# Kernel tuning notes

Measured on AMD Instinct MI355X. Metric: run time of the kernel, lower is better.

## Reference

```python
import jax, jax.numpy as jnp
import numpy as np

EPS = 1e-5

def _ln(z, g, b):
    # LayerNorm over last axis (per the gammas/betas of shape (2, 3H))
    mu = jnp.mean(z, axis=-1, keepdims=True)
    var = jnp.var(z, axis=-1, keepdims=True)
    return g * (z - mu) * jax.lax.rsqrt(var + EPS) + b

def setup_inputs() -> dict:
    key = jax.random.key(0)
    ks = jax.random.split(key, 12)
    B, L, D_IN, H, A, DEPTH = 64, 512, 256, 256, 128, 4
    glorot = lambda k, sh: jax.random.normal(k, sh, jnp.float32) * np.sqrt(2.0 / (sh[0] + sh[1])).astype(np.float32)
    # variable-length prefix masks (bucketing/masking semantics of the layer)
    lengths = jax.random.randint(ks[0], (B, 1), L // 2, L + 1)
    mask = jnp.arange(L)[None, :] < lengths
    return {
        'x': jax.random.normal(ks[1], (B, L, D_IN), jnp.float32),
        'mask': mask,
        'W_emb': glorot(ks[2], (D_IN, H)),
        'b_emb': jnp.zeros((H,), jnp.float32),
        'W': glorot(ks[3], (H, 3 * H)),
        'U': glorot(ks[4], (H, 3 * H)),
        'b': jnp.zeros((3 * H,), jnp.float32),
        'W_action_1': glorot(ks[5], (H, A)),
        'U_action_1': glorot(ks[6], (H, A)),
        'b_action_1': jnp.zeros((A,), jnp.float32),
        'W_action_2': glorot(ks[7], (A, 2)),
        'b_action_2': jnp.zeros((2,), jnp.float32),
        'gammas': jnp.ones((2, 3 * H), jnp.float32),
        'betas': jnp.zeros((2, 3 * H), jnp.float32),
        'depth': DEPTH,
    }

def _run_depth(x_seq, m_seq, W, U, b, Wa1, Ua1, ba1, Wa2, ba2, gammas, betas):
    # x_seq: (L,B,H), m_seq: (L,B) bool
    H = W.shape[0]
    B = x_seq.shape[1]
    # precompute + layernorm the input projection for all steps (fusable)
    xp_all = _ln(jnp.einsum('lbh,hk->lbk', x_seq, W), gammas[0], betas[0])  # (L,B,3H)

    def step(h, inputs):
        xp, xt, mt = inputs  # (B,3H), (B,H), (B,)
        hp = _ln(h @ U, gammas[1], betas[1])
        r = jax.nn.sigmoid(xp[:, :H] + hp[:, :H] + b[:H])
        z = jax.nn.sigmoid(xp[:, H:2 * H] + hp[:, H:2 * H] + b[H:2 * H])
        hh = jnp.tanh(xp[:, 2 * H:] + r * hp[:, 2 * H:] + b[2 * H:])
        h_new = z * h + (1.0 - z) * hh
        # action-policy subnetwork (binary merge/propagate decision)
        logits = jnp.tanh(xt @ Wa1 + h @ Ua1 + ba1) @ Wa2 + ba2  # (B,2)
        pol = jax.nn.softmax(logits, axis=-1)
        act = (pol[:, 1] > pol[:, 0]) & mt
        h_out = jnp.where(mt[:, None], h_new, h)  # masked steps carry state
        return h_out, (h_out, act, pol)

    h0 = jnp.zeros((B, H), x_seq.dtype)
    _, (h_seq, act_seq, pol_seq) = jax.lax.scan(step, h0, (xp_all, x_seq, m_seq))
    return h_seq, act_seq, pol_seq

def reference(x, mask, W_emb, b_emb, W, U, b, W_action_1, U_action_1, b_action_1,
              W_action_2, b_action_2, gammas, betas, depth):
    # embedding projection, then time-major like the Theano scans
    h_seq = jnp.swapaxes(x @ W_emb + b_emb, 0, 1)  # (L,B,H)
    m_seq = jnp.swapaxes(mask, 0, 1)               # (L,B)
    actions, policies = [], []
    for _ in range(depth):  # vertical (tree-depth) scan: small fixed count
        h_new, act, pol = _run_depth(h_seq, m_seq, W, U, b,
                                     W_action_1, U_action_1, b_action_1,
                                     W_action_2, b_action_2, gammas, betas)
        actions.append(act)
        policies.append(pol)
        h_seq = h_new
        m_seq = m_seq & act  # tree collapse: only selected nodes survive upward
    output = h_seq[-1]  # (B,H) final hidden state of top layer
    action = jnp.stack(actions, 0).transpose(2, 0, 1)      # (B,depth,L)
    policy = jnp.stack(policies, 0).transpose(2, 0, 1, 3)  # (B,depth,L,2)
    return output, action, policy
```

## Files before the change

### kernel.cpp

```cpp
#include <hip/hip_runtime.h>
#include <hip/hip_bf16.h>
#include <math.h>

#define BB 64
#define LL 512
#define HH 256
#define H3 768
#define AA 128
#define NDEPTH 4
#define NROWS (LL*BB)

#define EXCH_U64_PER_CHAIN (2 * 3 * 256)

typedef float vf32x32 __attribute__((ext_vector_type(32)));

__global__ void maskcvt_kernel(const unsigned char* __restrict__ raw,
                               int* __restrict__ m)
{
    int i = blockIdx.x * blockDim.x + threadIdx.x;
    bool bytemode = (raw[1] == 1);
    int v;
    if (bytemode) v = raw[i] ? 1 : 0;
    else          v = (((const int*)raw)[i] != 0) ? 1 : 0;
    m[i] = v;
}

__global__ __launch_bounds__(512) void mkidx_kernel(
    const int* __restrict__ m,
    int* __restrict__ rowidx,
    int* __restrict__ nact)
{
    const int b    = blockIdx.x;
    const int tid  = threadIdx.x;
    const int lane = tid & 63;
    const int w    = tid >> 6;
    __shared__ int wcnt[8];
    int pred = m[b * LL + tid];
    unsigned long long bal = __ballot(pred != 0);
    int below = __popcll(bal & ((1ull << lane) - 1ull));
    if (lane == 63) wcnt[w] = __popcll(bal);
    __syncthreads();
    int woff = 0;
#pragma unroll
    for (int i = 0; i < 8; ++i) woff += (i < w) ? wcnt[i] : 0;
    if (pred) rowidx[b * LL + woff + below] = tid;
    if (tid == 511) nact[b] = woff + wcnt[7];
}

template<int MODE, int EPI>
__global__ __launch_bounds__(256) void gemm_kernel(
    const float* __restrict__ A, const float* __restrict__ Bm,
    const float* __restrict__ bias, const float* __restrict__ aux,
    float* __restrict__ C, int M, int N,
    const int* __restrict__ ridx, const int* __restrict__ nact)
{
    __shared__ float As[16][136];
    __shared__ float Bs[16][136];
    const int tid = threadIdx.x;
    const int tx = tid & 15, ty = tid >> 4;
    const int row0 = blockIdx.y * 128, col0 = blockIdx.x * 128;

    int arow0 = 0, arow1 = 0;
    if (MODE == 3) {
        const int bb = row0 >> 9;
        const int na = nact[bb];
        if ((row0 & 511) >= na) return;
        const int r0 = row0 + (tid >> 2);
        const int r1 = r0 + 64;
        const int l0 = ((r0 & 511) < na) ? ridx[r0] : 0;
        const int l1 = ((r1 & 511) < na) ? ridx[r1] : 0;
        arow0 = l0 * 64 + bb;
        arow1 = l1 * 64 + bb;
    }

    float acc[8][8];
#pragma unroll
    for (int i = 0; i < 8; ++i)
#pragma unroll
        for (int j = 0; j < 8; ++j) acc[i][j] = 0.f;

    for (int kk = 0; kk < 256; kk += 16) {
#pragma unroll
        for (int i = 0; i < 2; ++i) {
            int aid = i * 256 + tid;
            int r   = aid >> 2;
            int k4  = (aid & 3) << 2;
            int rr  = row0 + r;
            float4 v;
            if (MODE == 0) {
                v = *(const float4*)(A + rr * 256 + kk + k4);
            } else if (MODE == 1) {
                v = *(const float4*)(A + (rr & 63) * 131072 + (rr >> 6) * 256 + kk + k4);
            } else if (MODE == 2) {
                if (rr < 64) v = make_float4(0.f, 0.f, 0.f, 0.f);
                else         v = *(const float4*)(A + (rr - 64) * 256 + kk + k4);
            } else {
                int ar = i ? arow1 : arow0;
                v = *(const float4*)(A + ar * 256 + kk + k4);
            }
            As[k4 + 0][r] = v.x; As[k4 + 1][r] = v.y;
            As[k4 + 2][r] = v.z; As[k4 + 3][r] = v.w;

            int bid = i * 256 + tid;
            int bk  = bid >> 5;
            int c4  = (bid & 31) << 2;
            float4 w = *(const float4*)(Bm + (kk + bk) * N + col0 + c4);
            *(float4*)&Bs[bk][c4] = w;
        }
        __syncthreads();
#pragma unroll
        for (int k = 0; k < 16; ++k) {
            float a[8], bb2[8];
            *(float4*)&a[0]   = *(const float4*)&As[k][ty * 8];
            *(float4*)&a[4]   = *(const float4*)&As[k][ty * 8 + 4];
            *(float4*)&bb2[0] = *(const float4*)&Bs[k][tx * 8];
            *(float4*)&bb2[4] = *(const float4*)&Bs[k][tx * 8 + 4];
#pragma unroll
            for (int i = 0; i < 8; ++i)
#pragma unroll
                for (int j = 0; j < 8; ++j)
                    acc[i][j] += a[i] * bb2[j];
        }
        __syncthreads();
    }

#pragma unroll
    for (int i = 0; i < 8; ++i) {
        int row  = row0 + ty * 8 + i;
        int colb = col0 + tx * 8;
        float vout[8];
#pragma unroll
        for (int j = 0; j < 8; ++j) {
            float v = acc[i][j];
            if (EPI == 1) v += bias[colb + j];
            if (EPI == 2) v = tanhf(v + aux[row * N + colb + j]);
            vout[j] = v;
        }
        *(float4*)&C[row * N + colb]     = *(float4*)&vout[0];
        *(float4*)&C[row * N + colb + 4] = *(float4*)&vout[4];
    }
}

__global__ __launch_bounds__(256) void lnrows_kernel(
    float* __restrict__ XP, const float* __restrict__ g0,
    const float* __restrict__ b0, const float* __restrict__ gb,
    const int* __restrict__ nact)
{
    const int row = blockIdx.x;
    if ((row & 511) >= nact[row >> 9]) return;
    const int tid = threadIdx.x;
    float* p = XP + (long)row * H3;
    float v0 = p[tid], v1 = p[tid + 256], v2 = p[tid + 512];
    float s = v0 + v1 + v2;
    float q = v0 * v0 + v1 * v1 + v2 * v2;
#pragma unroll
    for (int off = 32; off >= 1; off >>= 1) {
        s += __shfl_xor(s, off);
        q += __shfl_xor(q, off);
    }
    __shared__ float rs4[4], rq4[4];
    if ((tid & 63) == 0) { rs4[tid >> 6] = s; rq4[tid >> 6] = q; }
    __syncthreads();
    float S = rs4[0] + rs4[1] + rs4[2] + rs4[3];
    float Q = rq4[0] + rq4[1] + rq4[2] + rq4[3];
    float mu  = S * (1.f / 768.f);
    float var = Q * (1.f / 768.f) - mu * mu;
    float r   = rsqrtf(var + 1e-5f);
    p[tid]       = g0[tid]       * (v0 - mu) * r + b0[tid]       + gb[tid];
    p[tid + 256] = g0[tid + 256] * (v1 - mu) * r + b0[tid + 256] + gb[tid + 256];
    p[tid + 512] = g0[tid + 512] * (v2 - mu) * r + b0[tid + 512] + gb[tid + 512];
}

__global__ __launch_bounds__(512, 2) void scan3_kernel(
    const float* __restrict__ XP,
    const float* __restrict__ U,
    const float* __restrict__ g1, const float* __restrict__ b1,
    const int* __restrict__ mask,
    float* __restrict__ Y,
    unsigned long long* __restrict__ exch,
    int seq0)
{
    const int i0   = blockIdx.x;
    const int xcd  = i0 & 7;
    const int slot = i0 >> 3;
    const int b    = xcd + 8 * (slot / 3);
    const int s    = slot % 3;
    const int tid  = threadIdx.x;
    const int kg   = tid >> 5;
    const int cg   = tid & 31;
    const int q1   = (s + 1 >= 3) ? s - 2 : s + 1;
    const int q2   = (s + 2 >= 3) ? s - 1 : s + 2;

    __shared__ float h_cur[256];
    __shared__ float part[16][256];
    __shared__ float xp_lds[768];
    __shared__ float g1s[768], b1s[768];
    __shared__ int   mk[512];
    __shared__ float reds[4], redq[4];

    vf32x32 u0v, u1v, u2v, u3v;
    {
        const volatile float* Uv = U;
        const int colbase = s * 256 + cg;
#pragma unroll
        for (int i = 0; i < 16; ++i) {
#pragma unroll
            for (int j = 0; j < 8; ++j) {
                const int f = i * 8 + j;
                float val = Uv[(kg * 16 + i) * H3 + colbase + 32 * j];
                if      (f < 32) u0v[f]      = val;
                else if (f < 64) u1v[f - 32] = val;
                else if (f < 96) u2v[f - 64] = val;
                else             u3v[f - 96] = val;
            }
        }
    }
    if (tid < 256) h_cur[tid] = 0.f;
    for (int i = tid; i < 768; i += 512) { g1s[i] = g1[i]; b1s[i] = b1[i]; }
    mk[tid] = mask[b * LL + tid];
    __syncthreads();

    unsigned long long* exb = exch + b * EXCH_U64_PER_CHAIN;
    int seq = seq0;

    for (int l = 0; l < LL; ++l) {
        if (!mk[l]) {
            if (s == 0 && tid < 64) {
                float4 hv = *(const float4*)&h_cur[tid * 4];
                *(float4*)&Y[((long)l * BB + b) * HH + tid * 4] = hv;
            }
            continue;
        }
        seq++;
        const int par = seq & 1;
        const int cs  = seq - seq0 - 1;

        float4 xr4;
        if (tid < 192) xr4 = *(const float4*)(XP + ((long)(b * LL + cs)) * H3 + tid * 4);

        float acc[8] = {0.f, 0.f, 0.f, 0.f, 0.f, 0.f, 0.f, 0.f};
#pragma unroll
        for (int i = 0; i < 4; ++i) {
            float4 hv = *(const float4*)&h_cur[kg * 16 + i * 4];
#pragma unroll
            for (int e = 0; e < 4; ++e) {
                const float hh = (e == 0) ? hv.x : (e == 1) ? hv.y
                               : (e == 2) ? hv.z : hv.w;
                const int ik = i * 4 + e;
#pragma unroll
                for (int j = 0; j < 8; ++j) {
                    const int f = ik * 8 + j;
                    const float uu = (f < 32) ? u0v[f]
                                   : (f < 64) ? u1v[f - 32]
                                   : (f < 96) ? u2v[f - 64]
                                   :            u3v[f - 96];
                    acc[j] += uu * hh;
                }
            }
        }
#pragma unroll
        for (int j = 0; j < 8; ++j)
            part[kg][cg + 32 * j] = acc[j];
        __syncthreads();

        if (tid < 192) *(float4*)&xp_lds[tid * 4] = xr4;

        float pre = 0.f, v0 = 0.f, v1 = 0.f, v2 = 0.f;
        if (tid < 256) {
            pre = part[0][tid];
#pragma unroll
            for (int gg = 1; gg < 16; ++gg) pre += part[gg][tid];

            unsigned long long pk =
                ((unsigned long long)(unsigned)seq << 32) |
                (unsigned long long)__float_as_uint(pre);
            __hip_atomic_store(&exb[(par * 3 + s) * 256 + tid], pk,
                               __ATOMIC_RELAXED, __HIP_MEMORY_SCOPE_AGENT);

            unsigned long long x1 = 0, x2 = 0;
            bool d1 = false, d2 = false;
            do {
                unsigned long long t1 =
                    __hip_atomic_load(&exb[(par * 3 + q1) * 256 + tid],
                                      __ATOMIC_RELAXED, __HIP_MEMORY_SCOPE_AGENT);
                unsigned long long t2 =
                    __hip_atomic_load(&exb[(par * 3 + q2) * 256 + tid],
                                      __ATOMIC_RELAXED, __HIP_MEMORY_SCOPE_AGENT);
                if (!d1 && (int)(t1 >> 32) == seq) { x1 = t1; d1 = true; }
                if (!d2 && (int)(t2 >> 32) == seq) { x2 = t2; d2 = true; }
            } while (!(d1 && d2));
            float w1 = __uint_as_float((unsigned)x1);
            float w2 = __uint_as_float((unsigned)x2);
            v0 = (s == 0) ? pre : ((q1 == 0) ? w1 : w2);
            v1 = (s == 1) ? pre : ((q1 == 1) ? w1 : w2);
            v2 = (s == 2) ? pre : ((q1 == 2) ? w1 : w2);

            float st = v0 + v1 + v2;
            float qt = v0 * v0 + v1 * v1 + v2 * v2;
#pragma unroll
            for (int off = 32; off >= 1; off >>= 1) {
                st += __shfl_xor(st, off);
                qt += __shfl_xor(qt, off);
            }
            if ((tid & 63) == 0) { reds[tid >> 6] = st; redq[tid >> 6] = qt; }
        }
        __syncthreads();

        if (tid < 256) {
            float S = reds[0] + reds[1] + reds[2] + reds[3];
            float Q = redq[0] + redq[1] + redq[2] + redq[3];
            float mu = S * (1.f / 768.f);
            float rs = rsqrtf(Q * (1.f / 768.f) - mu * mu + 1e-5f);
            float hp_r = g1s[tid]       * (v0 - mu) * rs + b1s[tid];
            float hp_z = g1s[256 + tid] * (v1 - mu) * rs + b1s[256 + tid];
            float hp_h = g1s[512 + tid] * (v2 - mu) * rs + b1s[512 + tid];
            float xr = xp_lds[tid], xz = xp_lds[256 + tid], xh = xp_lds[512 + tid];
            float r  = 1.f / (1.f + expf(-(xr + hp_r)));
            float z  = 1.f / (1.f + expf(-(xz + hp_z)));
            float hh = tanhf(xh + r * hp_h);
            float o  = z * h_cur[tid] + (1.f - z) * hh;
            h_cur[tid] = o;
            if (s == 0) Y[((long)l * BB + b) * HH + tid] = o;
        }
        __syncthreads();
    }
}

__global__ __launch_bounds__(256) void act_kernel(
    const float* __restrict__ T, const float* __restrict__ Wa2,
    const float* __restrict__ ba2, const int* __restrict__ mask_in,
    int* __restrict__ mask_out, float* __restrict__ act_out,
    float* __restrict__ pol_out, int d)
{
    int row  = blockIdx.x * 4 + (threadIdx.x >> 6);
    int lane = threadIdx.x & 63;
    const float* Tr = T + (long)row * AA;
    float t0 = Tr[lane], t1 = Tr[lane + 64];
    float l0 = t0 * Wa2[lane * 2]       + t1 * Wa2[(lane + 64) * 2];
    float l1 = t0 * Wa2[lane * 2 + 1]   + t1 * Wa2[(lane + 64) * 2 + 1];
#pragma unroll
    for (int off = 32; off >= 1; off >>= 1) {
        l0 += __shfl_xor(l0, off);
        l1 += __shfl_xor(l1, off);
    }
    if (lane == 0) {
        int l = row >> 6, bb = row & 63;
        l0 += ba2[0]; l1 += ba2[1];
        float m  = fmaxf(l0, l1);
        float e0 = expf(l0 - m), e1 = expf(l1 - m);
        float inv = 1.f / (e0 + e1);
        float p0 = e0 * inv, p1 = e1 * inv;
        int mt = mask_in[bb * LL + l];
        int a  = (p1 > p0) && mt;
        act_out[bb * (NDEPTH * LL) + d * LL + l] = a ? 1.f : 0.f;
        pol_out[bb * (NDEPTH * LL * 2) + d * (LL * 2) + l * 2 + 0] = p0;
        pol_out[bb * (NDEPTH * LL * 2) + d * (LL * 2) + l * 2 + 1] = p1;
        mask_out[bb * LL + l] = a;
    }
}

__global__ void final_copy_kernel(const float* __restrict__ X, float* __restrict__ out)
{
    int i = blockIdx.x * blockDim.x + threadIdx.x;
    int bb = i >> 8, j = i & 255;
    out[i] = X[((long)(LL - 1) * BB + bb) * HH + j];
}

extern "C" void kernel_launch(void* const* d_in, const int* in_sizes, int n_in,
                              void* d_out, int out_size, void* d_ws, size_t ws_size,
                              hipStream_t stream)
{
    const float* x      = (const float*)d_in[0];
    const void*  mraw   = d_in[1];
    const float* W_emb  = (const float*)d_in[2];
    const float* b_emb  = (const float*)d_in[3];
    const float* W      = (const float*)d_in[4];
    const float* U      = (const float*)d_in[5];
    const float* bias3  = (const float*)d_in[6];
    const float* Wa1    = (const float*)d_in[7];
    const float* Ua1    = (const float*)d_in[8];
    const float* ba1    = (const float*)d_in[9];
    const float* Wa2    = (const float*)d_in[10];
    const float* ba2    = (const float*)d_in[11];
    const float* gammas = (const float*)d_in[12];
    const float* betas  = (const float*)d_in[13];

    float* out = (float*)d_out;
    char*  ws  = (char*)d_ws;

    float* XP = (float*)(ws);
    float* X  = (float*)(ws + 100663296UL);
    float* Y  = (float*)(ws + 134217728UL);
    float* XA = (float*)(ws + 167772160UL);
    float* T  = XP;
    int*   m0 = (int*)(ws + 184549376UL);
    int*   m1 = (int*)(ws + 184680448UL);

    float* act_out = out + BB * HH;
    float* pol_out = act_out + BB * NDEPTH * LL;

    maskcvt_kernel<<<dim3(NROWS / 256), dim3(256), 0, stream>>>(
        (const unsigned char*)mraw, m0);

    gemm_kernel<1, 1><<<dim3(2, 256), dim3(256), 0, stream>>>(
        x, W_emb, b_emb, nullptr, X, NROWS, HH, nullptr, nullptr);

    float* Xc = X; float* Yc = Y;
    int* mc = m0; int* mn = m1;

    for (int d = 0; d < NDEPTH; ++d) {
        int* rowidx = (int*)Yc;
        int* nactp  = ((int*)Yc) + NROWS;

        mkidx_kernel<<<dim3(BB), dim3(512), 0, stream>>>(mc, rowidx, nactp);

        gemm_kernel<3, 0><<<dim3(6, 256), dim3(256), 0, stream>>>(
            Xc, W, nullptr, nullptr, XP, NROWS, H3, rowidx, nactp);
        lnrows_kernel<<<dim3(NROWS), dim3(256), 0, stream>>>(
            XP, gammas, betas, bias3, nactp);

        gemm_kernel<0, 1><<<dim3(1, 256), dim3(256), 0, stream>>>(
            Xc, Wa1, ba1, nullptr, XA, NROWS, AA, nullptr, nullptr);

        unsigned long long* exch_d = (unsigned long long*)Xc;

        scan3_kernel<<<dim3(192), dim3(512), 0, stream>>>(
            XP, U, gammas + H3, betas + H3, mc, Yc, exch_d, d << 10);

        gemm_kernel<2, 2><<<dim3(1, 256), dim3(256), 0, stream>>>(
            Yc, Ua1, nullptr, XA, T, NROWS, AA, nullptr, nullptr);
        act_kernel<<<dim3(NROWS / 4), dim3(256), 0, stream>>>(
            T, Wa2, ba2, mc, mn, act_out, pol_out, d);
        { float* tmp = Xc; Xc = Yc; Yc = tmp; }
        { int* tmp = mc; mc = mn; mn = tmp; }
    }

    final_copy_kernel<<<dim3(BB), dim3(256), 0, stream>>>(Xc, out);
}
```

Before: 3.398 ms.

## Overlap Wa1 projection with scan blocks; fuse Ua1 GEMM with action softmax

The Wa1 input projection moves into extra blocks of the scan kernel, so it runs on compute units left idle by the 192 recurrent blocks. The Ua1 GEMM is fused with the tanh/Wa2/softmax action epilogue, which removes the intermediate T buffer and a separate kernel launch. The exchange buffer gets its own workspace region because Xc is now read by the side GEMM blocks, and the spin-wait adds s_sleep backoff. Risks: the extra blocks could compete with the persistent scan blocks for residency or memory bandwidth, and the backoff could add latency to each step's exchange.

```diff
diff --git a/kernel.cpp b/kernel.cpp
--- a/kernel.cpp
+++ b/kernel.cpp
@@ -50,7 +50,7 @@
 template<int MODE, int EPI>
 __global__ __launch_bounds__(256) void gemm_kernel(
     const float* __restrict__ A, const float* __restrict__ Bm,
-    const float* __restrict__ bias, const float* __restrict__ aux,
+    const float* __restrict__ bias,
     float* __restrict__ C, int M, int N,
     const int* __restrict__ ridx, const int* __restrict__ nact)
 {
@@ -87,13 +87,8 @@
             int k4  = (aid & 3) << 2;
             int rr  = row0 + r;
             float4 v;
-            if (MODE == 0) {
-                v = *(const float4*)(A + rr * 256 + kk + k4);
-            } else if (MODE == 1) {
+            if (MODE == 1) {
                 v = *(const float4*)(A + (rr & 63) * 131072 + (rr >> 6) * 256 + kk + k4);
-            } else if (MODE == 2) {
-                if (rr < 64) v = make_float4(0.f, 0.f, 0.f, 0.f);
-                else         v = *(const float4*)(A + (rr - 64) * 256 + kk + k4);
             } else {
                 int ar = i ? arow1 : arow0;
                 v = *(const float4*)(A + ar * 256 + kk + k4);
@@ -133,7 +128,6 @@
         for (int j = 0; j < 8; ++j) {
             float v = acc[i][j];
             if (EPI == 1) v += bias[colb + j];
-            if (EPI == 2) v = tanhf(v + aux[row * N + colb + j]);
             vout[j] = v;
         }
         *(float4*)&C[row * N + colb]     = *(float4*)&vout[0];
@@ -178,25 +172,85 @@
     const int* __restrict__ mask,
     float* __restrict__ Y,
     unsigned long long* __restrict__ exch,
-    int seq0)
-{
-    const int i0   = blockIdx.x;
-    const int xcd  = i0 & 7;
-    const int slot = i0 >> 3;
-    const int b    = xcd + 8 * (slot / 3);
-    const int s    = slot % 3;
-    const int tid  = threadIdx.x;
-    const int kg   = tid >> 5;
-    const int cg   = tid & 31;
-    const int q1   = (s + 1 >= 3) ? s - 2 : s + 1;
-    const int q2   = (s + 2 >= 3) ? s - 1 : s + 2;
-
+    int seq0,
+    const float* __restrict__ Xc,
+    const float* __restrict__ Wa1,
+    const float* __restrict__ ba1,
+    float* __restrict__ XA)
+{
     __shared__ float h_cur[256];
     __shared__ float part[16][256];
     __shared__ float xp_lds[768];
     __shared__ float g1s[768], b1s[768];
     __shared__ int   mk[512];
     __shared__ float reds[4], redq[4];
+    __shared__ float As[16][136];
+    __shared__ float Bs[16][136];
+
+    const int tid = threadIdx.x;
+
+    if (blockIdx.x >= 192) {
+        const int t    = blockIdx.x - 192;
+        const int row0 = t * 128;
+        const int tx   = tid & 15;
+        const int ty4  = tid >> 4;
+        float xacc[4][8];
+#pragma unroll
+        for (int i = 0; i < 4; ++i)
+#pragma unroll
+            for (int j = 0; j < 8; ++j) xacc[i][j] = 0.f;
+
+        for (int kk = 0; kk < 256; kk += 16) {
+            {
+                int r  = tid >> 2;
+                int k4 = (tid & 3) << 2;
+                float4 v = *(const float4*)(Xc + (row0 + r) * 256 + kk + k4);
+                As[k4 + 0][r] = v.x; As[k4 + 1][r] = v.y;
+                As[k4 + 2][r] = v.z; As[k4 + 3][r] = v.w;
+            }
+            {
+                int bk = tid >> 5;
+                int c4 = (tid & 31) << 2;
+                float4 w = *(const float4*)(Wa1 + (kk + bk) * AA + c4);
+                *(float4*)&Bs[bk][c4] = w;
+            }
+            __syncthreads();
+#pragma unroll
+            for (int k = 0; k < 16; ++k) {
+                float a[4], bb2[8];
+                *(float4*)&a[0]   = *(const float4*)&As[k][ty4 * 4];
+                *(float4*)&bb2[0] = *(const float4*)&Bs[k][tx * 8];
+                *(float4*)&bb2[4] = *(const float4*)&Bs[k][tx * 8 + 4];
+#pragma unroll
+                for (int i = 0; i < 4; ++i)
+#pragma unroll
+                    for (int j = 0; j < 8; ++j)
+                        xacc[i][j] += a[i] * bb2[j];
+            }
+            __syncthreads();
+        }
+#pragma unroll
+        for (int i = 0; i < 4; ++i) {
+            int row  = row0 + ty4 * 4 + i;
+            int colb = tx * 8;
+            float vout[8];
+#pragma unroll
+            for (int j = 0; j < 8; ++j) vout[j] = xacc[i][j] + ba1[colb + j];
+            *(float4*)&XA[row * AA + colb]     = *(float4*)&vout[0];
+            *(float4*)&XA[row * AA + colb + 4] = *(float4*)&vout[4];
+        }
+        return;
+    }
+
+    const int i0   = blockIdx.x;
+    const int xcd  = i0 & 7;
+    const int slot = i0 >> 3;
+    const int b    = xcd + 8 * (slot / 3);
+    const int s    = slot % 3;
+    const int kg   = tid >> 5;
+    const int cg   = tid & 31;
+    const int q1   = (s + 1 >= 3) ? s - 2 : s + 1;
+    const int q2   = (s + 2 >= 3) ? s - 1 : s + 2;
 
     vf32x32 u0v, u1v, u2v, u3v;
     {
@@ -279,6 +333,7 @@
 
             unsigned long long x1 = 0, x2 = 0;
             bool d1 = false, d2 = false;
+            int spins = 0;
             do {
                 unsigned long long t1 =
                     __hip_atomic_load(&exb[(par * 3 + q1) * 256 + tid],
@@ -288,6 +343,7 @@
                                       __ATOMIC_RELAXED, __HIP_MEMORY_SCOPE_AGENT);
                 if (!d1 && (int)(t1 >> 32) == seq) { x1 = t1; d1 = true; }
                 if (!d2 && (int)(t2 >> 32) == seq) { x2 = t2; d2 = true; }
+                if (++spins > 8) __builtin_amdgcn_s_sleep(1);
             } while (!(d1 && d2));
             float w1 = __uint_as_float((unsigned)x1);
             float w2 = __uint_as_float((unsigned)x2);
@@ -326,36 +382,103 @@
     }
 }
 
-__global__ __launch_bounds__(256) void act_kernel(
-    const float* __restrict__ T, const float* __restrict__ Wa2,
-    const float* __restrict__ ba2, const int* __restrict__ mask_in,
-    int* __restrict__ mask_out, float* __restrict__ act_out,
-    float* __restrict__ pol_out, int d)
-{
-    int row  = blockIdx.x * 4 + (threadIdx.x >> 6);
-    int lane = threadIdx.x & 63;
-    const float* Tr = T + (long)row * AA;
-    float t0 = Tr[lane], t1 = Tr[lane + 64];
-    float l0 = t0 * Wa2[lane * 2]       + t1 * Wa2[(lane + 64) * 2];
-    float l1 = t0 * Wa2[lane * 2 + 1]   + t1 * Wa2[(lane + 64) * 2 + 1];
-#pragma unroll
-    for (int off = 32; off >= 1; off >>= 1) {
-        l0 += __shfl_xor(l0, off);
-        l1 += __shfl_xor(l1, off);
-    }
-    if (lane == 0) {
-        int l = row >> 6, bb = row & 63;
-        l0 += ba2[0]; l1 += ba2[1];
-        float m  = fmaxf(l0, l1);
-        float e0 = expf(l0 - m), e1 = expf(l1 - m);
-        float inv = 1.f / (e0 + e1);
-        float p0 = e0 * inv, p1 = e1 * inv;
-        int mt = mask_in[bb * LL + l];
-        int a  = (p1 > p0) && mt;
-        act_out[bb * (NDEPTH * LL) + d * LL + l] = a ? 1.f : 0.f;
-        pol_out[bb * (NDEPTH * LL * 2) + d * (LL * 2) + l * 2 + 0] = p0;
-        pol_out[bb * (NDEPTH * LL * 2) + d * (LL * 2) + l * 2 + 1] = p1;
-        mask_out[bb * LL + l] = a;
+__global__ __launch_bounds__(256) void gemmact_kernel(
+    const float* __restrict__ Yprev,
+    const float* __restrict__ Ua1,
+    const float* __restrict__ XA,
+    const float* __restrict__ Wa2,
+    const float* __restrict__ ba2,
+    const int* __restrict__ mask_in, int* __restrict__ mask_out,
+    float* __restrict__ act_out, float* __restrict__ pol_out, int d)
+{
+    __shared__ float As[16][136];
+    __shared__ float Bs[16][136];
+    const int tid = threadIdx.x;
+    const int tx = tid & 15, ty = tid >> 4;
+    const int row0 = blockIdx.y * 128;
+
+    float acc[8][8];
+#pragma unroll
+    for (int i = 0; i < 8; ++i)
+#pragma unroll
+        for (int j = 0; j < 8; ++j) acc[i][j] = 0.f;
+
+    for (int kk = 0; kk < 256; kk += 16) {
+#pragma unroll
+        for (int i = 0; i < 2; ++i) {
+            int aid = i * 256 + tid;
+            int r   = aid >> 2;
+            int k4  = (aid & 3) << 2;
+            int rr  = row0 + r;
+            float4 v;
+            if (rr < 64) v = make_float4(0.f, 0.f, 0.f, 0.f);
+            else         v = *(const float4*)(Yprev + (rr - 64) * 256 + kk + k4);
+            As[k4 + 0][r] = v.x; As[k4 + 1][r] = v.y;
+            As[k4 + 2][r] = v.z; As[k4 + 3][r] = v.w;
+
+            int bid = i * 256 + tid;
+            int bk  = bid >> 5;
+            int c4  = (bid & 31) << 2;
+            float4 w = *(const float4*)(Ua1 + (kk + bk) * AA + c4);
+            *(float4*)&Bs[bk][c4] = w;
+        }
+        __syncthreads();
+#pragma unroll
+        for (int k = 0; k < 16; ++k) {
+            float a[8], bb2[8];
+            *(float4*)&a[0]   = *(const float4*)&As[k][ty * 8];
+            *(float4*)&a[4]   = *(const float4*)&As[k][ty * 8 + 4];
+            *(float4*)&bb2[0] = *(const float4*)&Bs[k][tx * 8];
+            *(float4*)&bb2[4] = *(const float4*)&Bs[k][tx * 8 + 4];
+#pragma unroll
+            for (int i = 0; i < 8; ++i)
+#pragma unroll
+                for (int j = 0; j < 8; ++j)
+                    acc[i][j] += a[i] * bb2[j];
+        }
+        __syncthreads();
+    }
+
+    float p0[8], p1[8];
+#pragma unroll
+    for (int i = 0; i < 8; ++i) { p0[i] = 0.f; p1[i] = 0.f; }
+#pragma unroll
+    for (int i = 0; i < 8; ++i) {
+        int row  = row0 + ty * 8 + i;
+#pragma unroll
+        for (int j = 0; j < 8; ++j) {
+            int c   = tx * 8 + j;
+            float v = tanhf(acc[i][j] + XA[row * AA + c]);
+            p0[i] += v * Wa2[c * 2];
+            p1[i] += v * Wa2[c * 2 + 1];
+        }
+    }
+#pragma unroll
+    for (int off = 1; off < 16; off <<= 1) {
+#pragma unroll
+        for (int i = 0; i < 8; ++i) {
+            p0[i] += __shfl_xor(p0[i], off);
+            p1[i] += __shfl_xor(p1[i], off);
+        }
+    }
+    if (tx == 0) {
+#pragma unroll
+        for (int i = 0; i < 8; ++i) {
+            int row = row0 + ty * 8 + i;
+            int l   = row >> 6, bb = row & 63;
+            float l0 = p0[i] + ba2[0];
+            float l1 = p1[i] + ba2[1];
+            float m  = fmaxf(l0, l1);
+            float e0 = expf(l0 - m), e1 = expf(l1 - m);
+            float inv = 1.f / (e0 + e1);
+            float q0 = e0 * inv, q1v = e1 * inv;
+            int mt = mask_in[bb * LL + l];
+            int a  = (q1v > q0) && mt;
+            act_out[bb * (NDEPTH * LL) + d * LL + l] = a ? 1.f : 0.f;
+            pol_out[bb * (NDEPTH * LL * 2) + d * (LL * 2) + l * 2 + 0] = q0;
+            pol_out[bb * (NDEPTH * LL * 2) + d * (LL * 2) + l * 2 + 1] = q1v;
+            mask_out[bb * LL + l] = a;
+        }
     }
 }
 
@@ -392,9 +515,9 @@
     float* X  = (float*)(ws + 100663296UL);
     float* Y  = (float*)(ws + 134217728UL);
     float* XA = (float*)(ws + 167772160UL);
-    float* T  = XP;
     int*   m0 = (int*)(ws + 184549376UL);
     int*   m1 = (int*)(ws + 184680448UL);
+    unsigned long long* exch_d = (unsigned long long*)(ws + 184811520UL);
 
     float* act_out = out + BB * HH;
     float* pol_out = act_out + BB * NDEPTH * LL;
@@ -403,7 +526,7 @@
         (const unsigned char*)mraw, m0);
 
     gemm_kernel<1, 1><<<dim3(2, 256), dim3(256), 0, stream>>>(
-        x, W_emb, b_emb, nullptr, X, NROWS, HH, nullptr, nullptr);
+        x, W_emb, b_emb, X, NROWS, HH, nullptr, nullptr);
 
     float* Xc = X; float* Yc = Y;
     int* mc = m0; int* mn = m1;
@@ -415,22 +538,17 @@
         mkidx_kernel<<<dim3(BB), dim3(512), 0, stream>>>(mc, rowidx, nactp);
 
         gemm_kernel<3, 0><<<dim3(6, 256), dim3(256), 0, stream>>>(
-            Xc, W, nullptr, nullptr, XP, NROWS, H3, rowidx, nactp);
+            Xc, W, nullptr, XP, NROWS, H3, rowidx, nactp);
         lnrows_kernel<<<dim3(NROWS), dim3(256), 0, stream>>>(
             XP, gammas, betas, bias3, nactp);
 
-        gemm_kernel<0, 1><<<dim3(1, 256), dim3(256), 0, stream>>>(
-            Xc, Wa1, ba1, nullptr, XA, NROWS, AA, nullptr, nullptr);
-
-        unsigned long long* exch_d = (unsigned long long*)Xc;
-
-        scan3_kernel<<<dim3(192), dim3(512), 0, stream>>>(
-            XP, U, gammas + H3, betas + H3, mc, Yc, exch_d, d << 10);
-
-        gemm_kernel<2, 2><<<dim3(1, 256), dim3(256), 0, stream>>>(
-            Yc, Ua1, nullptr, XA, T, NROWS, AA, nullptr, nullptr);
-        act_kernel<<<dim3(NROWS / 4), dim3(256), 0, stream>>>(
-            T, Wa2, ba2, mc, mn, act_out, pol_out, d);
+        scan3_kernel<<<dim3(448), dim3(512), 0, stream>>>(
+            XP, U, gammas + H3, betas + H3, mc, Yc, exch_d, d << 10,
+            Xc, Wa1, ba1, XA);
+
+        gemmact_kernel<<<dim3(1, 256), dim3(256), 0, stream>>>(
+            Yc, Ua1, XA, Wa2, ba2, mc, mn, act_out, pol_out, d);
+
         { float* tmp = Xc; Xc = Yc; Yc = tmp; }
         { int* tmp = mc; mc = mn; mn = tmp; }
     }
```

After: 3.295 ms, median of 2. -3.0%, faster.
